# Performance work log

Measured on AMD Instinct MI355X. Metric: run time of the kernel, lower is better.

Reference implementation:

```python
import jax, jax.numpy as jnp
import numpy as np

B, C, S = 128, 32, 512          # batch, input_channel, seq_len (= d_model of the encoders)
EMB = 256                       # embed_size
NHEAD = 8                       # args.num_heads (also TransformerEncoderLayer nhead)
DFF = 2048                      # torch TransformerEncoderLayer default dim_feedforward
RLEN = S // 2 + 1               # 257 rfft bins
HK = int(RLEN * 0.5)            # 128, 'hight_freq_k' split point
LK = RLEN - HK                  # 129

def _ln(x, w, b, axes=-1):
    m = jnp.mean(x, axis=axes, keepdims=True)
    v = jnp.var(x, axis=axes, keepdims=True)
    return (x - m) / jnp.sqrt(v + 1e-5) * w + b

def _tel(x, in_w, in_b, out_w, out_b, ln1w, ln1b, w1, b1, w2, b2, ln2w, ln2b):
    # torch nn.TransformerEncoderLayer (batch_first, post-norm, relu, eval-mode dropout)
    b_, s_, d_ = x.shape
    dh = d_ // NHEAD
    qkv = x @ in_w.T + in_b
    q, k, v = jnp.split(qkv, 3, axis=-1)
    sp = lambda t: t.reshape(b_, s_, NHEAD, dh).transpose(0, 2, 1, 3)
    q, k, v = sp(q), sp(k), sp(v)
    sc = jnp.einsum('bhqd,bhkd->bhqk', q, k) / jnp.sqrt(jnp.asarray(dh, x.dtype))
    att = jax.nn.softmax(sc, axis=-1)
    o = jnp.einsum('bhqk,bhkd->bhqd', att, v).transpose(0, 2, 1, 3).reshape(b_, s_, d_)
    o = o @ out_w.T + out_b
    x = _ln(x + o, ln1w, ln1b)
    f = jax.nn.relu(x @ w1.T + b1) @ w2.T + b2
    return _ln(x + f, ln2w, ln2b)

def _crelu(z):
    return jax.lax.complex(jax.nn.relu(z.real), jax.nn.relu(z.imag))

def _csoftmax(z):
    return jax.lax.complex(jax.nn.softmax(z.real, axis=-1), jax.nn.softmax(z.imag, axis=-1))

def _cattn(q):
    # self-attention with complex Q=K=V (no conjugate, per torch matmul(Q, K^T))
    dk = q.shape[-1]
    sc = jnp.einsum('bqe,bke->bqk', q, q) / jnp.asarray(dk, jnp.float32) ** 0.5
    return jnp.einsum('bqk,bke->bqe', _csoftmax(sc), q)

def setup_inputs() -> dict:
    key = jax.random.key(0)
    ks = iter(jax.random.split(key, 64))
    n = lambda *sh: jax.random.normal(next(ks), sh, jnp.float32) * 0.02
    d = {'x': jax.random.normal(next(ks), (B, C, S), jnp.float32)}
    for p in ('t', 'r'):
        d[p + '_in_w'] = n(3 * S, S);  d[p + '_in_b'] = jnp.zeros((3 * S,), jnp.float32)
        d[p + '_out_w'] = n(S, S);     d[p + '_out_b'] = jnp.zeros((S,), jnp.float32)
        d[p + '_ln1_w'] = jnp.ones((S,), jnp.float32); d[p + '_ln1_b'] = jnp.zeros((S,), jnp.float32)
        d[p + '_lin1_w'] = n(DFF, S); d[p + '_lin1_b'] = jnp.zeros((DFF,), jnp.float32)
        d[p + '_lin2_w'] = n(S, DFF); d[p + '_lin2_b'] = jnp.zeros((S,), jnp.float32)
        d[p + '_ln2_w'] = jnp.ones((S,), jnp.float32); d[p + '_ln2_b'] = jnp.zeros((S,), jnp.float32)
    d['lc_w'] = n(S, S);  d['lc_b'] = jnp.zeros((S,), jnp.float32)
    d['up1_w'] = n(S, S); d['up1_b'] = jnp.zeros((S,), jnp.float32)
    d['up2_w'] = n(S, S); d['up2_b'] = jnp.zeros((S,), jnp.float32)
    d['n1_w'] = jnp.ones((C, S), jnp.float32); d['n1_b'] = jnp.zeros((C, S), jnp.float32)
    d['n2_w'] = jnp.ones((C, S), jnp.float32); d['n2_b'] = jnp.zeros((C, S), jnp.float32)
    d['l1_re'] = jax.random.normal(next(ks), (HK, EMB), jnp.float32)
    d['l1_im'] = jax.random.normal(next(ks), (HK, EMB), jnp.float32)
    d['h1_re'] = jax.random.normal(next(ks), (LK, EMB), jnp.float32)
    d['h1_im'] = jax.random.normal(next(ks), (LK, EMB), jnp.float32)
    d['lb1_re'] = jax.random.normal(next(ks), (EMB,), jnp.float32)
    d['lb1_im'] = jax.random.normal(next(ks), (EMB,), jnp.float32)
    d['hb1_re'] = jax.random.normal(next(ks), (EMB,), jnp.float32)
    d['hb1_im'] = jax.random.normal(next(ks), (EMB,), jnp.float32)
    return d

def reference(x, t_in_w, t_in_b, t_out_w, t_out_b, t_ln1_w, t_ln1_b, t_lin1_w, t_lin1_b, t_lin2_w, t_lin2_b, t_ln2_w, t_ln2_b, r_in_w, r_in_b, r_out_w, r_out_b, r_ln1_w, r_ln1_b, r_lin1_w, r_lin1_b, r_lin2_w, r_lin2_b, r_ln2_w, r_ln2_b, lc_w, lc_b, up1_w, up1_b, up2_w, up2_b, n1_w, n1_b, n2_w, n2_b, l1_re, l1_im, h1_re, h1_im, lb1_re, lb1_im, hb1_re, hb1_im):
    l1 = jax.lax.complex(l1_re, l1_im)
    h1 = jax.lax.complex(h1_re, h1_im)
    lb1 = jax.lax.complex(lb1_re, lb1_im)
    hb1 = jax.lax.complex(hb1_re, hb1_im)
    down_x = x  # downsample_scale=1 and padding_length=0 -> identity (i=0 path)
    # main branch
    df = jax.nn.relu(_tel(down_x, t_in_w, t_in_b, t_out_w, t_out_b, t_ln1_w, t_ln1_b,
                          t_lin1_w, t_lin1_b, t_lin2_w, t_lin2_b, t_ln2_w, t_ln2_b))
    df = _ln(df, n1_w, n1_b, axes=(-2, -1))
    # ttf_freqaug
    xf = jnp.fft.rfft(down_x, norm='ortho')                      # [B, C, 257] complex
    low = _crelu(jnp.einsum('bdk,ke->bde', xf[..., :HK], l1) + lb1)
    high = _crelu(jnp.einsum('bdk,ke->bde', xf[..., HK:], h1) + hb1)
    low = low + _cattn(low)
    high = high + _cattn(high)
    xcat = jnp.concatenate([low, high[..., low.shape[-1]:]], axis=-1)  # EMB bins (high slice is empty)
    fa = jnp.fft.irfft(xcat, n=S, norm='ortho')                  # zero-pads 256 -> 257 bins
    fa = fa @ lc_w.T + lc_b                                      # linear_change
    up = (fa @ up1_w.T + up1_b) @ up2_w.T + up2_b                # linear_up_sampling
    # recons branch
    rf = jax.nn.relu(_tel(fa, r_in_w, r_in_b, r_out_w, r_out_b, r_ln1_w, r_ln1_b,
                          r_lin1_w, r_lin1_b, r_lin2_w, r_lin2_b, r_ln2_w, r_ln2_b))
    rf = _ln(rf, n2_w, n2_b, axes=(-2, -1))
    res = df + rf
    return (res, down_x, fa, up)
```

## Files before the change

### kernel.cpp

```cpp
#include <hip/hip_runtime.h>
#include <math.h>


#define NROW 4096
#define NOUT 2097152

typedef __attribute__((ext_vector_type(8))) short short8;
typedef __attribute__((ext_vector_type(4))) float floatx4;

__device__ __forceinline__ unsigned short f2bf(float f) {
    union { float f; unsigned u; } v; v.f = f;
    return (unsigned short)((v.u + 0x7fffu + ((v.u >> 16) & 1u)) >> 16);
}
__device__ __forceinline__ float bf2f(unsigned short h) {
    union { unsigned u; float f; } v; v.u = ((unsigned)h) << 16;
    return v.f;
}

__device__ __forceinline__ void gload16(const unsigned short* g, unsigned short* l) {
    __builtin_amdgcn_global_load_lds((const __attribute__((address_space(1))) void*)g,
                                     (__attribute__((address_space(3))) void*)l, 16, 0, 0);
}

__device__ __forceinline__ void xcd_swizzle(int& bx, int& by, int& bz) {
    const int gx = gridDim.x, gy = gridDim.y;
    const int nwg = gx * gy * gridDim.z;
    int b = (bz * gy + by) * gx + bx;
    const int chunk = nwg >> 3;
    const int lb = (b & 7) * chunk + (b >> 3);
    bx = lb % gx;
    const int rem = lb / gx;
    by = rem % gy;
    bz = rem / gy;
}

__global__ __launch_bounds__(256) void tab_kernel(float* __restrict__ tabC, float* __restrict__ tabS)
{
    int n = blockIdx.x, k = threadIdx.x;
    int m = (n * k) & 511;
    float th = (float)m * 0.01227184630308513f;
    float s, c; sincosf(th, &s, &c);
    tabC[n * 256 + k] = c;
    tabS[n * 256 + k] = s;
}

__global__ __launch_bounds__(256) void wa_kernel(const float* __restrict__ l1_re, const float* __restrict__ l1_im,
                                                 const float* __restrict__ tabC, const float* __restrict__ tabS,
                                                 float* __restrict__ Wa)
{
    int n  = blockIdx.x;
    int ep = blockIdx.y * 256 + threadIdx.x;
    const float inv = 0.04419417382415922f;
    float acc = 0.f;
    if (ep < 256) {
        for (int k = 0; k < 128; ++k) {
            float c = tabC[n * 256 + k], s = tabS[n * 256 + k];
            acc += c * l1_re[k * 256 + ep] + s * l1_im[k * 256 + ep];
        }
    } else {
        int e = ep - 256;
        for (int k = 0; k < 128; ++k) {
            float c = tabC[n * 256 + k], s = tabS[n * 256 + k];
            acc += c * l1_im[k * 256 + e] - s * l1_re[k * 256 + e];
        }
    }
    Wa[(size_t)ep * 512 + n] = acc * inv;
}

__global__ __launch_bounds__(256) void wm_kernel(const float* __restrict__ lc_w,
                                                 const float* __restrict__ tabC, const float* __restrict__ tabS,
                                                 float* __restrict__ Wm)
{
    __shared__ float lw[512];
    int s  = blockIdx.x;
    int kk = blockIdx.y * 256 + threadIdx.x;
    for (int i = threadIdx.x; i < 512; i += 256) lw[i] = lc_w[s * 512 + i];
    __syncthreads();
    const float inv = 0.04419417382415922f;
    float acc = 0.f;
    if (kk < 256) {
        int k = kk;
        for (int n = 0; n < 512; ++n) acc += tabC[n * 256 + k] * lw[n];
        acc *= (k == 0) ? inv : 2.f * inv;
    } else {
        int k = kk - 256;
        if (k == 0) acc = 0.f;
        else {
            for (int n = 0; n < 512; ++n) acc += tabS[n * 256 + k] * lw[n];
            acc *= -2.f * inv;
        }
    }
    Wm[(size_t)s * 512 + kk] = acc;
}

__global__ __launch_bounds__(256) void lbpack_kernel(const float* __restrict__ re, const float* __restrict__ im,
                                                     float* __restrict__ out)
{
    int i = threadIdx.x + blockIdx.x * 256;
    if (i < 512) out[i] = (i < 256) ? re[i] : im[i - 256];
}

__global__ __launch_bounds__(256) void wcvt_kernel(
    const float* s0, const float* s1, const float* s2, const float* s3, const float* s4,
    const float* s5, const float* s6, const float* s7, const float* s8, const float* s9,
    unsigned short* __restrict__ o)
{
    int i = blockIdx.x * 256 + threadIdx.x;
    if (i >= 6815744) return;
    const float* s; int off;
    if (i < 3145728) {
        if (i < 1048576) { if (i < 786432) { s = s0; off = 0; } else { s = s1; off = 786432; } }
        else             { if (i < 2097152) { s = s2; off = 1048576; } else { s = s3; off = 2097152; } }
    } else {
        if (i < 5242880) {
            if (i < 3932160) { s = s4; off = 3145728; }
            else if (i < 4194304) { s = s5; off = 3932160; }
            else { s = s6; off = 4194304; }
        } else {
            if (i < 6291456) { s = s7; off = 5242880; }
            else if (i < 6553600) { s = s8; off = 6291456; }
            else { s = s9; off = 6553600; }
        }
    }
    o[i] = f2bf(s[i - off]);
}

__global__ __launch_bounds__(256) void cvt_hilo_kernel(const float* __restrict__ a, unsigned short* __restrict__ hi,
                                                       unsigned short* __restrict__ lo, int n)
{
    for (int i = blockIdx.x * 256 + threadIdx.x; i < n; i += gridDim.x * 256) {
        unsigned short h = f2bf(a[i]);
        hi[i] = h;
        lo[i] = f2bf(a[i] - bf2f(h));
    }
}
__global__ __launch_bounds__(256) void cvt_lo_kernel(const float* __restrict__ a, const unsigned short* __restrict__ hi,
                                                     unsigned short* __restrict__ lo, int n)
{
    for (int i = blockIdx.x * 256 + threadIdx.x; i < n; i += gridDim.x * 256)
        lo[i] = f2bf(a[i] - bf2f(hi[i]));
}

__global__ __launch_bounds__(256) void xsplit_kernel(const float* __restrict__ a, unsigned short* __restrict__ hi,
                                                     unsigned short* __restrict__ lo, float* __restrict__ cp, int n)
{
    for (int i = blockIdx.x * 256 + threadIdx.x; i < n; i += gridDim.x * 256) {
        float v = a[i];
        unsigned short h = f2bf(v);
        hi[i] = h;
        lo[i] = f2bf(v - bf2f(h));
        cp[i] = v;
    }
}

template <int TM, int TN, int ACT, int WF, int WBF>
__global__ __launch_bounds__(256) void gemm_mfma(
    const unsigned short* __restrict__ A, const unsigned short* __restrict__ W,
    const float* __restrict__ bias, float* __restrict__ Cf,
    unsigned short* __restrict__ Cb, int N, int K)
{
    constexpr int MI = TM / 32, NJ = TN / 32;
    constexpr int ARW = TM / 4, BRW = TN / 4;
    __shared__ unsigned short As[2][TM * 32];
    __shared__ unsigned short Bs[2][TN * 32];
    const int tid = threadIdx.x;
    const int wave = tid >> 6, lane = tid & 63;
    int bx = blockIdx.x, by = blockIdx.y, bz = blockIdx.z;
    xcd_swizzle(bx, by, bz);
    const int m0 = by * TM, n0 = bx * TN;
    const int sr = lane >> 2, sc = (lane & 3) * 8;
    const unsigned short* aS = A + (size_t)(m0 + wave * ARW + sr) * K + sc;
    const unsigned short* wS = W + (size_t)(n0 + wave * BRW + sr) * K + sc;
    const int wm = (wave >> 1) * (TM / 2), wn = (wave & 1) * (TN / 2);
    const int fr = lane & 15, fko = (lane >> 4) * 8;

    floatx4 acc[MI][NJ];
#pragma unroll
    for (int i = 0; i < MI; ++i)
#pragma unroll
        for (int j = 0; j < NJ; ++j) acc[i][j] = (floatx4){0.f, 0.f, 0.f, 0.f};

    for (int k0 = 0; k0 < K; k0 += 64) {
#pragma unroll
        for (int h = 0; h < 2; ++h) {
#pragma unroll
            for (int c = 0; c < ARW / 16; ++c)
                gload16(aS + (size_t)(16 * c) * K + k0 + 32 * h, &As[h][(wave * ARW + 16 * c) * 32]);
#pragma unroll
            for (int c = 0; c < BRW / 16; ++c)
                gload16(wS + (size_t)(16 * c) * K + k0 + 32 * h, &Bs[h][(wave * BRW + 16 * c) * 32]);
        }
        __syncthreads();
#pragma unroll
        for (int h = 0; h < 2; ++h) {
            short8 af[MI], bfr[NJ];
#pragma unroll
            for (int i = 0; i < MI; ++i) af[i] = *(const short8*)&As[h][(wm + i * 16 + fr) * 32 + fko];
#pragma unroll
            for (int j = 0; j < NJ; ++j) bfr[j] = *(const short8*)&Bs[h][(wn + j * 16 + fr) * 32 + fko];
#pragma unroll
            for (int i = 0; i < MI; ++i)
#pragma unroll
                for (int j = 0; j < NJ; ++j)
                    acc[i][j] = __builtin_amdgcn_mfma_f32_16x16x32_bf16(af[i], bfr[j], acc[i][j], 0, 0, 0);
        }
        __syncthreads();
    }
    const int r0 = m0 + wm + (lane >> 4) * 4;
#pragma unroll
    for (int i = 0; i < MI; ++i) {
#pragma unroll
        for (int j = 0; j < NJ; ++j) {
            int n = n0 + wn + j * 16 + fr;
            float bv = bias[n];
#pragma unroll
            for (int r = 0; r < 4; ++r) {
                int m = r0 + i * 16 + r;
                size_t idx = (size_t)m * N + n;
                float v = acc[i][j][r] + bv;
                if (ACT) v = fmaxf(v, 0.f);
                if (WF) Cf[idx] = v;
                if (WBF) Cb[idx] = f2bf(v);
            }
        }
    }
}

template <int TM, int TN, int ACT, int WBF>
__global__ __launch_bounds__(256) void gemm_dual(
    const unsigned short* __restrict__ A0, const unsigned short* __restrict__ A1,
    const unsigned short* __restrict__ W0, const unsigned short* __restrict__ W1,
    const float* __restrict__ b0, const float* __restrict__ b1,
    float* __restrict__ C0, float* __restrict__ C1,
    unsigned short* __restrict__ D0, unsigned short* __restrict__ D1, int N, int K)
{
    constexpr int MI = TM / 32, NJ = TN / 32;
    constexpr int ARW = TM / 4, BRW = TN / 4;
    __shared__ unsigned short As[2][TM * 32];
    __shared__ unsigned short Bs[2][TN * 32];
    const int tid = threadIdx.x;
    const int wave = tid >> 6, lane = tid & 63;
    int bx = blockIdx.x, by = blockIdx.y, bz = blockIdx.z;
    xcd_swizzle(bx, by, bz);
    const int m0 = by * TM, n0 = bx * TN;
    const int z = bz;
    const unsigned short* A = z ? A1 : A0;
    const unsigned short* W = z ? W1 : W0;
    const float* bias = z ? b1 : b0;
    float* Cf = z ? C1 : C0;
    unsigned short* Cb = z ? D1 : D0;
    const int sr = lane >> 2, sc = (lane & 3) * 8;
    const unsigned short* aS = A + (size_t)(m0 + wave * ARW + sr) * K + sc;
    const unsigned short* wS = W + (size_t)(n0 + wave * BRW + sr) * K + sc;
    const int wm = (wave >> 1) * (TM / 2), wn = (wave & 1) * (TN / 2);
    const int fr = lane & 15, fko = (lane >> 4) * 8;

    floatx4 acc[MI][NJ];
#pragma unroll
    for (int i = 0; i < MI; ++i)
#pragma unroll
        for (int j = 0; j < NJ; ++j) acc[i][j] = (floatx4){0.f, 0.f, 0.f, 0.f};

    for (int k0 = 0; k0 < K; k0 += 64) {
#pragma unroll
        for (int h = 0; h < 2; ++h) {
#pragma unroll
            for (int c = 0; c < ARW / 16; ++c)
                gload16(aS + (size_t)(16 * c) * K + k0 + 32 * h, &As[h][(wave * ARW + 16 * c) * 32]);
#pragma unroll
            for (int c = 0; c < BRW / 16; ++c)
                gload16(wS + (size_t)(16 * c) * K + k0 + 32 * h, &Bs[h][(wave * BRW + 16 * c) * 32]);
        }
        __syncthreads();
#pragma unroll
        for (int h = 0; h < 2; ++h) {
            short8 af[MI], bfr[NJ];
#pragma unroll
            for (int i = 0; i < MI; ++i) af[i] = *(const short8*)&As[h][(wm + i * 16 + fr) * 32 + fko];
#pragma unroll
            for (int j = 0; j < NJ; ++j) bfr[j] = *(const short8*)&Bs[h][(wn + j * 16 + fr) * 32 + fko];
#pragma unroll
            for (int i = 0; i < MI; ++i)
#pragma unroll
                for (int j = 0; j < NJ; ++j)
                    acc[i][j] = __builtin_amdgcn_mfma_f32_16x16x32_bf16(af[i], bfr[j], acc[i][j], 0, 0, 0);
        }
        __syncthreads();
    }
    const int r0 = m0 + wm + (lane >> 4) * 4;
#pragma unroll
    for (int i = 0; i < MI; ++i) {
#pragma unroll
        for (int j = 0; j < NJ; ++j) {
            int n = n0 + wn + j * 16 + fr;
            float bv = bias[n];
#pragma unroll
            for (int r = 0; r < 4; ++r) {
                int m = r0 + i * 16 + r;
                size_t idx = (size_t)m * N + n;
                float v = acc[i][j][r] + bv;
                if (ACT) v = fmaxf(v, 0.f);
                if (WBF) Cb[idx] = f2bf(v);
                else     Cf[idx] = v;
            }
        }
    }
}

template <int TM, int TN, int ACT, int WCOPY, int WHILO>
__global__ __launch_bounds__(256) void gemm_mfma3(
    const unsigned short* __restrict__ Ah, const unsigned short* __restrict__ Al,
    const unsigned short* __restrict__ Wh, const unsigned short* __restrict__ Wl,
    const float* __restrict__ bias, float* __restrict__ Cf, float* __restrict__ Ccopy,
    unsigned short* __restrict__ Hh, unsigned short* __restrict__ Hl, int N, int K)
{
    constexpr int MI = TM / 32, NJ = TN / 32;
    constexpr int ARW = TM / 4, BRW = TN / 4;
    __shared__ unsigned short Ash[2][TM * 32];
    __shared__ unsigned short Asl[2][TM * 32];
    __shared__ unsigned short Bsh[2][TN * 32];
    __shared__ unsigned short Bsl[2][TN * 32];
    const int tid = threadIdx.x;
    const int wave = tid >> 6, lane = tid & 63;
    int bx = blockIdx.x, by = blockIdx.y, bz = blockIdx.z;
    xcd_swizzle(bx, by, bz);
    const int m0 = by * TM, n0 = bx * TN;
    const int sr = lane >> 2, sc = (lane & 3) * 8;
    const size_t aoff = (size_t)(m0 + wave * ARW + sr) * K + sc;
    const size_t woff = (size_t)(n0 + wave * BRW + sr) * K + sc;
    const int wm = (wave >> 1) * (TM / 2), wn = (wave & 1) * (TN / 2);
    const int fr = lane & 15, fko = (lane >> 4) * 8;

    floatx4 acc[MI][NJ];
#pragma unroll
    for (int i = 0; i < MI; ++i)
#pragma unroll
        for (int j = 0; j < NJ; ++j) acc[i][j] = (floatx4){0.f, 0.f, 0.f, 0.f};

    for (int k0 = 0; k0 < K; k0 += 64) {
#pragma unroll
        for (int h = 0; h < 2; ++h) {
#pragma unroll
            for (int c = 0; c < ARW / 16; ++c) {
                gload16(Ah + aoff + (size_t)(16 * c) * K + k0 + 32 * h, &Ash[h][(wave * ARW + 16 * c) * 32]);
                gload16(Al + aoff + (size_t)(16 * c) * K + k0 + 32 * h, &Asl[h][(wave * ARW + 16 * c) * 32]);
            }
#pragma unroll
            for (int c = 0; c < BRW / 16; ++c) {
                gload16(Wh + woff + (size_t)(16 * c) * K + k0 + 32 * h, &Bsh[h][(wave * BRW + 16 * c) * 32]);
                gload16(Wl + woff + (size_t)(16 * c) * K + k0 + 32 * h, &Bsl[h][(wave * BRW + 16 * c) * 32]);
            }
        }
        __syncthreads();
#pragma unroll
        for (int h = 0; h < 2; ++h) {
            short8 ah[MI], al[MI], bh[NJ], bl[NJ];
#pragma unroll
            for (int i = 0; i < MI; ++i) {
                ah[i] = *(const short8*)&Ash[h][(wm + i * 16 + fr) * 32 + fko];
                al[i] = *(const short8*)&Asl[h][(wm + i * 16 + fr) * 32 + fko];
            }
#pragma unroll
            for (int j = 0; j < NJ; ++j) {
                bh[j] = *(const short8*)&Bsh[h][(wn + j * 16 + fr) * 32 + fko];
                bl[j] = *(const short8*)&Bsl[h][(wn + j * 16 + fr) * 32 + fko];
            }
#pragma unroll
            for (int i = 0; i < MI; ++i)
#pragma unroll
                for (int j = 0; j < NJ; ++j) {
                    acc[i][j] = __builtin_amdgcn_mfma_f32_16x16x32_bf16(al[i], bh[j], acc[i][j], 0, 0, 0);
                    acc[i][j] = __builtin_amdgcn_mfma_f32_16x16x32_bf16(ah[i], bl[j], acc[i][j], 0, 0, 0);
                    acc[i][j] = __builtin_amdgcn_mfma_f32_16x16x32_bf16(ah[i], bh[j], acc[i][j], 0, 0, 0);
                }
        }
        __syncthreads();
    }
    const int r0 = m0 + wm + (lane >> 4) * 4;
#pragma unroll
    for (int i = 0; i < MI; ++i) {
#pragma unroll
        for (int j = 0; j < NJ; ++j) {
            int n = n0 + wn + j * 16 + fr;
            float bv = bias[n];
#pragma unroll
            for (int r = 0; r < 4; ++r) {
                int m = r0 + i * 16 + r;
                size_t idx = (size_t)m * N + n;
                float v = acc[i][j][r] + bv;
                if (ACT) v = fmaxf(v, 0.f);
                Cf[idx] = v;
                if (WCOPY) Ccopy[idx] = v;
                if (WHILO) {
                    unsigned short h = f2bf(v);
                    Hh[idx] = h;
                    Hl[idx] = f2bf(v - bf2f(h));
                }
            }
        }
    }
}

__global__ __launch_bounds__(256) void attn_dual_kernel(const float* __restrict__ qkvF,
                                                        const unsigned short* __restrict__ qkvB,
                                                        unsigned short* __restrict__ outR,
                                                        unsigned short* __restrict__ outT)
{
    const int isT = blockIdx.x >> 10;
    const int bid = blockIdx.x & 1023;
    const int b = bid >> 3;
    const int h = bid & 7;
    __shared__ float qs[32][65], ks[32][65], vs[32][65];
    __shared__ float ps[32][33];
    const int tid = threadIdx.x;
    if (isT) {
        for (int i = tid; i < 2048; i += 256) {
            int s = i >> 6, d = i & 63;
            size_t base = ((size_t)(b * 32 + s)) * 1536 + h * 64 + d;
            qs[s][d] = bf2f(qkvB[base]);
            ks[s][d] = bf2f(qkvB[base + 512]);
            vs[s][d] = bf2f(qkvB[base + 1024]);
        }
    } else {
        for (int i = tid; i < 2048; i += 256) {
            int s = i >> 6, d = i & 63;
            size_t base = ((size_t)(b * 32 + s)) * 1536 + h * 64 + d;
            qs[s][d] = qkvF[base];
            ks[s][d] = qkvF[base + 512];
            vs[s][d] = qkvF[base + 1024];
        }
    }
    __syncthreads();
    for (int i = tid; i < 1024; i += 256) {
        int si = i >> 5, sj = i & 31;
        float acc = 0.f;
#pragma unroll 8
        for (int d = 0; d < 64; ++d) acc += qs[si][d] * ks[sj][d];
        ps[si][sj] = acc * 0.125f;
    }
    __syncthreads();
    if (tid < 32) {
        float mx = -1e30f;
        for (int j = 0; j < 32; ++j) mx = fmaxf(mx, ps[tid][j]);
        float sum = 0.f;
        for (int j = 0; j < 32; ++j) { float e = __expf(ps[tid][j] - mx); ps[tid][j] = e; sum += e; }
        float inv = 1.f / sum;
        for (int j = 0; j < 32; ++j) ps[tid][j] *= inv;
    }
    __syncthreads();
    unsigned short* ob = isT ? outT : outR;
    for (int i = tid; i < 2048; i += 256) {
        int s = i >> 6, d = i & 63;
        float acc = 0.f;
#pragma unroll 8
        for (int k = 0; k < 32; ++k) acc += ps[s][k] * vs[k][d];
        ob[((size_t)(b * 32 + s)) * 512 + h * 64 + d] = f2bf(acc);
    }
}

__global__ __launch_bounds__(512) void cattn2_kernel(const float* __restrict__ LL,
                                                     unsigned short* __restrict__ outHi,
                                                     unsigned short* __restrict__ outLo)
{
    extern __shared__ float Xs[];
    __shared__ float Pr[16][33], Pi[16][33];
    const int b = blockIdx.x, half = blockIdx.y;
    const int tid = threadIdx.x;
    const float* base = LL + (size_t)b * 16384;
    for (int i = tid; i < 16384; i += 512) {
        int c = i >> 9, e = i & 511;
        Xs[e * 32 + ((c ^ e) & 31)] = base[i];
    }
    __syncthreads();
    {
        const int li = tid >> 5;
        const int ci = half * 16 + li;
        const int ck = tid & 31;
        float ar = 0.f, ai = 0.f;
#pragma unroll 4
        for (int er = 0; er < 256; ++er) {
            const int sw = er & 31;
            float yr = Xs[er * 32 + ((ck ^ sw) & 31)];
            float yi = Xs[(er + 256) * 32 + ((ck ^ sw) & 31)];
            float xr = Xs[er * 32 + ((ci ^ sw) & 31)];
            float xi = Xs[(er + 256) * 32 + ((ci ^ sw) & 31)];
            ar += xr * yr - xi * yi;
            ai += xr * yi + xi * yr;
        }
        Pr[li][ck] = ar * 0.0625f;
        Pi[li][ck] = ai * 0.0625f;
    }
    __syncthreads();
    if (tid < 32) {
        int r = tid & 15;
        float (*P)[33] = (tid < 16) ? Pr : Pi;
        float mx = -1e30f;
        for (int j = 0; j < 32; ++j) mx = fmaxf(mx, P[r][j]);
        float s = 0.f;
        for (int j = 0; j < 32; ++j) { float e = __expf(P[r][j] - mx); P[r][j] = e; s += e; }
        float inv = 1.f / s;
        for (int j = 0; j < 32; ++j) P[r][j] *= inv;
    }
    __syncthreads();
    const int er = tid & 255;
    const int th = tid >> 8;
    const int sw = er & 31;
    float accr[8], acci[8];
#pragma unroll
    for (int t = 0; t < 8; ++t) { accr[t] = 0.f; acci[t] = 0.f; }
    for (int k = 0; k < 32; ++k) {
        float yr = Xs[er * 32 + ((k ^ sw) & 31)];
        float yi = Xs[(er + 256) * 32 + ((k ^ sw) & 31)];
#pragma unroll
        for (int t = 0; t < 8; ++t) {
            float pr = Pr[th * 8 + t][k], pi = Pi[th * 8 + t][k];
            accr[t] += pr * yr - pi * yi;
            acci[t] += pr * yi + pi * yr;
        }
    }
#pragma unroll
    for (int t = 0; t < 8; ++t) {
        int c = half * 16 + th * 8 + t;
        float vr = Xs[er * 32 + ((c ^ sw) & 31)] + accr[t];
        float vi = Xs[(er + 256) * 32 + ((c ^ sw) & 31)] + acci[t];
        size_t ir = (size_t)b * 16384 + (size_t)c * 512 + er;
        unsigned short hr = f2bf(vr), hi2 = f2bf(vi);
        outHi[ir] = hr;        outLo[ir] = f2bf(vr - bf2f(hr));
        outHi[ir + 256] = hi2; outLo[ir + 256] = f2bf(vi - bf2f(hi2));
    }
}

__global__ __launch_bounds__(256) void add_ln_d1(
    const float* __restrict__ r0, const float* __restrict__ y0,
    const float* __restrict__ w0, const float* __restrict__ b0,
    unsigned short* __restrict__ h0, unsigned short* __restrict__ l0,
    const float* __restrict__ r1, const float* __restrict__ y1,
    const float* __restrict__ w1, const float* __restrict__ b1,
    unsigned short* __restrict__ h1, unsigned short* __restrict__ l1)
{
    const int row = blockIdx.x;
    const int br = row >> 12;
    const int rl = row & 4095;
    const float* resid = br ? r1 : r0;
    const float* y     = br ? y1 : y0;
    const float* w     = br ? w1 : w0;
    const float* bb    = br ? b1 : b0;
    unsigned short* oh = br ? h1 : h0;
    unsigned short* ol = br ? l1 : l0;
    const int tid = threadIdx.x;
    const size_t base = (size_t)rl * 512;
    float v0 = resid[base + tid] + y[base + tid];
    float v1 = resid[base + 256 + tid] + y[base + 256 + tid];
    float s = v0 + v1, q = v0 * v0 + v1 * v1;
    for (int off = 32; off; off >>= 1) { s += __shfl_down(s, off); q += __shfl_down(q, off); }
    __shared__ float sw[4], qw[4], ms, is;
    int wid = tid >> 6, lane = tid & 63;
    if (lane == 0) { sw[wid] = s; qw[wid] = q; }
    __syncthreads();
    if (tid == 0) {
        float S = sw[0] + sw[1] + sw[2] + sw[3];
        float Q = qw[0] + qw[1] + qw[2] + qw[3];
        float m = S * (1.f / 512.f);
        ms = m;
        is = rsqrtf(Q * (1.f / 512.f) - m * m + 1e-5f);
    }
    __syncthreads();
    float m = ms, inv = is;
    float o0 = (v0 - m) * inv * w[tid] + bb[tid];
    float o1 = (v1 - m) * inv * w[256 + tid] + bb[256 + tid];
    unsigned short e0 = f2bf(o0), e1 = f2bf(o1);
    oh[base + tid] = e0;       ol[base + tid] = f2bf(o0 - bf2f(e0));
    oh[base + 256 + tid] = e1; ol[base + 256 + tid] = f2bf(o1 - bf2f(e1));
}

__global__ __launch_bounds__(256) void add_ln_d2(
    const unsigned short* __restrict__ rh0, const unsigned short* __restrict__ rl0,
    const float* __restrict__ y0, const float* __restrict__ w0, const float* __restrict__ b0,
    float* __restrict__ o0p,
    const unsigned short* __restrict__ rh1, const unsigned short* __restrict__ rl1,
    const float* __restrict__ y1, const float* __restrict__ w1, const float* __restrict__ b1,
    float* __restrict__ o1p)
{
    const int row = blockIdx.x;
    const int br = row >> 12;
    const int rl = row & 4095;
    const unsigned short* rh = br ? rh1 : rh0;
    const unsigned short* rlo = br ? rl1 : rl0;
    const float* y  = br ? y1 : y0;
    const float* w  = br ? w1 : w0;
    const float* bb = br ? b1 : b0;
    float* op = br ? o1p : o0p;
    const int tid = threadIdx.x;
    const size_t base = (size_t)rl * 512;
    float v0 = bf2f(rh[base + tid]) + bf2f(rlo[base + tid]) + y[base + tid];
    float v1 = bf2f(rh[base + 256 + tid]) + bf2f(rlo[base + 256 + tid]) + y[base + 256 + tid];
    float s = v0 + v1, q = v0 * v0 + v1 * v1;
    for (int off = 32; off; off >>= 1) { s += __shfl_down(s, off); q += __shfl_down(q, off); }
    __shared__ float sw[4], qw[4], ms, is;
    int wid = tid >> 6, lane = tid & 63;
    if (lane == 0) { sw[wid] = s; qw[wid] = q; }
    __syncthreads();
    if (tid == 0) {
        float S = sw[0] + sw[1] + sw[2] + sw[3];
        float Q = qw[0] + qw[1] + qw[2] + qw[3];
        float m = S * (1.f / 512.f);
        ms = m;
        is = rsqrtf(Q * (1.f / 512.f) - m * m + 1e-5f);
    }
    __syncthreads();
    float m = ms, inv = is;
    op[base + tid]       = (v0 - m) * inv * w[tid] + bb[tid];
    op[base + 256 + tid] = (v1 - m) * inv * w[256 + tid] + bb[256 + tid];
}

template <int ADDF>
__global__ __launch_bounds__(256) void relu_bln_kernel(const float* __restrict__ xin,
                                                       const float* __restrict__ w, const float* __restrict__ b,
                                                       const float* __restrict__ addsrc,
                                                       float* __restrict__ out)
{
    const int bb = blockIdx.x;
    const int tid = threadIdx.x;
    const float* xp = xin + (size_t)bb * 16384;
    float s = 0.f, q = 0.f;
    for (int i = tid; i < 16384; i += 256) { float v = fmaxf(xp[i], 0.f); s += v; q += v * v; }
    for (int off = 32; off; off >>= 1) { s += __shfl_down(s, off); q += __shfl_down(q, off); }
    __shared__ float sw[4], qw[4], ms, is;
    int wid = tid >> 6, lane = tid & 63;
    if (lane == 0) { sw[wid] = s; qw[wid] = q; }
    __syncthreads();
    if (tid == 0) {
        float S = sw[0] + sw[1] + sw[2] + sw[3];
        float Q = qw[0] + qw[1] + qw[2] + qw[3];
        float m = S * (1.f / 16384.f);
        ms = m;
        is = rsqrtf(Q * (1.f / 16384.f) - m * m + 1e-5f);
    }
    __syncthreads();
    float m = ms, inv = is;
    const float* ap = ADDF ? (addsrc + (size_t)bb * 16384) : nullptr;
    float* op = out + (size_t)bb * 16384;
    for (int i = tid; i < 16384; i += 256) {
        float v = fmaxf(xp[i], 0.f);
        float o = (v - m) * inv * w[i] + b[i];
        if (ADDF) o += ap[i];
        op[i] = o;
    }
}

extern "C" void kernel_launch(void* const* d_in, const int* in_sizes, int n_in,
                              void* d_out, int out_size, void* d_ws, size_t ws_size,
                              hipStream_t stream)
{
    (void)in_sizes; (void)n_in; (void)out_size; (void)ws_size;
    const float* x        = (const float*)d_in[0];
    const float* t_in_w   = (const float*)d_in[1];
    const float* t_in_b   = (const float*)d_in[2];
    const float* t_out_w  = (const float*)d_in[3];
    const float* t_out_b  = (const float*)d_in[4];
    const float* t_ln1_w  = (const float*)d_in[5];
    const float* t_ln1_b  = (const float*)d_in[6];
    const float* t_lin1_w = (const float*)d_in[7];
    const float* t_lin1_b = (const float*)d_in[8];
    const float* t_lin2_w = (const float*)d_in[9];
    const float* t_lin2_b = (const float*)d_in[10];
    const float* t_ln2_w  = (const float*)d_in[11];
    const float* t_ln2_b  = (const float*)d_in[12];
    const float* r_in_w   = (const float*)d_in[13];
    const float* r_in_b   = (const float*)d_in[14];
    const float* r_out_w  = (const float*)d_in[15];
    const float* r_out_b  = (const float*)d_in[16];
    const float* r_ln1_w  = (const float*)d_in[17];
    const float* r_ln1_b  = (const float*)d_in[18];
    const float* r_lin1_w = (const float*)d_in[19];
    const float* r_lin1_b = (const float*)d_in[20];
    const float* r_lin2_w = (const float*)d_in[21];
    const float* r_lin2_b = (const float*)d_in[22];
    const float* r_ln2_w  = (const float*)d_in[23];
    const float* r_ln2_b  = (const float*)d_in[24];
    const float* lc_w     = (const float*)d_in[25];
    const float* lc_b     = (const float*)d_in[26];
    const float* up1_w    = (const float*)d_in[27];
    const float* up1_b    = (const float*)d_in[28];
    const float* up2_w    = (const float*)d_in[29];
    const float* up2_b    = (const float*)d_in[30];
    const float* n1_w     = (const float*)d_in[31];
    const float* n1_b     = (const float*)d_in[32];
    const float* n2_w     = (const float*)d_in[33];
    const float* n2_b     = (const float*)d_in[34];
    const float* l1_re    = (const float*)d_in[35];
    const float* l1_im    = (const float*)d_in[36];
    const float* lb1_re   = (const float*)d_in[39];
    const float* lb1_im   = (const float*)d_in[40];

    float* outp = (float*)d_out;

    float* WS   = (float*)d_ws;
    float* LL   = WS;
    float* FA   = WS;
    float* yR   = WS;
    float* QR   = WS + 2097152;
    float* tabC = QR;
    float* tabS = QR + 131072;
    float* WaF  = QR + 262144;
    float* WmF  = QR + 524288;
    unsigned short* WaHu = (unsigned short*)(QR + 786432);
    unsigned short* WaLu = (unsigned short*)(QR + 917504);
    unsigned short* WmHu = (unsigned short*)(QR + 1048576);
    unsigned short* WmLu = (unsigned short*)(QR + 1179648);
    float* qkvR = QR;
    unsigned short* x1rH = (unsigned short*)(WS + 2097152);
    unsigned short* x1rL = (unsigned short*)(WS + 3145728);
    unsigned short* x1tH = (unsigned short*)(WS + 4194304);
    unsigned short* x1tL = (unsigned short*)(WS + 5242880);
    float* yT   = WS + 6291456;
    unsigned short* qkvT = (unsigned short*)(WS + 8388608);
    unsigned short* f1R  = (unsigned short*)(WS + 8388608);
    float* x2R  = WS + 8388608;
    float* x2T  = WS + 10485760;
    unsigned short* xHi = (unsigned short*)(WS + 11534336);
    unsigned short* xLo = (unsigned short*)(WS + 12582912);
    unsigned short* aoR = (unsigned short*)(WS + 11534336);
    unsigned short* aoT = (unsigned short*)(WS + 12582912);
    unsigned short* f1T = (unsigned short*)(WS + 12582912);
    unsigned short* LLH = (unsigned short*)(WS + 13631488);
    unsigned short* LLL = (unsigned short*)(WS + 14680064);
    unsigned short* u1b = (unsigned short*)(WS + 13631488);
    float* oR   = WS + 13631488;
    float* oT   = WS + 15728640;
    unsigned short* faHi = (unsigned short*)(WS + 15728640);
    unsigned short* faLo = (unsigned short*)(WS + 16777216);
    unsigned short* rinLoU = (unsigned short*)(WS + 17825792);
    float* LB   = WS + 18219008;
    unsigned short* WB = (unsigned short*)(WS + 18366464);

    unsigned short* w_tin  = WB + 0;
    unsigned short* w_tout = WB + 786432;
    unsigned short* w_tl1  = WB + 1048576;
    unsigned short* w_tl2  = WB + 2097152;
    unsigned short* w_rin  = WB + 3145728;
    unsigned short* w_rout = WB + 3932160;
    unsigned short* w_rl1  = WB + 4194304;
    unsigned short* w_rl2  = WB + 5242880;
    unsigned short* w_up1  = WB + 6291456;
    unsigned short* w_up2  = WB + 6553600;

    dim3 blk(256);

    tab_kernel<<<dim3(512), blk, 0, stream>>>(tabC, tabS);
    wa_kernel<<<dim3(512, 2), blk, 0, stream>>>(l1_re, l1_im, tabC, tabS, WaF);
    wm_kernel<<<dim3(512, 2), blk, 0, stream>>>(lc_w, tabC, tabS, WmF);
    cvt_hilo_kernel<<<dim3(1024), blk, 0, stream>>>(WaF, WaHu, WaLu, 262144);
    cvt_hilo_kernel<<<dim3(1024), blk, 0, stream>>>(WmF, WmHu, WmLu, 262144);
    lbpack_kernel<<<dim3(2), blk, 0, stream>>>(lb1_re, lb1_im, LB);
    wcvt_kernel<<<dim3(26624), blk, 0, stream>>>(t_in_w, t_out_w, t_lin1_w, t_lin2_w,
                                                 r_in_w, r_out_w, r_lin1_w, r_lin2_w,
                                                 up1_w, up2_w, WB);
    xsplit_kernel<<<dim3(2048), blk, 0, stream>>>(x, xHi, xLo, outp + NOUT, NOUT);

    gemm_mfma3<64,64,1,0,0><<<dim3(8, 64), blk, 0, stream>>>(xHi, xLo, WaHu, WaLu, LB,
                                                             LL, nullptr, nullptr, nullptr, 512, 512);
    cattn2_kernel<<<dim3(128, 2), dim3(512), 65536, stream>>>(LL, LLH, LLL);
    gemm_mfma3<64,64,0,1,1><<<dim3(8, 64), blk, 0, stream>>>(LLH, LLL, WmHu, WmLu, lc_b,
                                                             FA, outp + 2 * NOUT, faHi, faLo, 512, 512);
    cvt_lo_kernel<<<dim3(768), blk, 0, stream>>>(r_in_w, w_rin, rinLoU, 786432);

    gemm_mfma<64,64,0,0,1><<<dim3(8, 64), blk, 0, stream>>>(faHi, w_up1, up1_b, nullptr, u1b, 512, 512);
    gemm_mfma<64,64,0,1,0><<<dim3(8, 64), blk, 0, stream>>>(u1b, w_up2, up2_b, outp + 3 * NOUT, nullptr, 512, 512);

    gemm_mfma3<64,128,0,0,0><<<dim3(12, 64), blk, 0, stream>>>(faHi, faLo, w_rin, rinLoU, r_in_b,
                                                               qkvR, nullptr, nullptr, nullptr, 1536, 512);
    gemm_mfma<64,128,0,0,1><<<dim3(12, 64), blk, 0, stream>>>(xHi, w_tin, t_in_b, nullptr, qkvT, 1536, 512);

    attn_dual_kernel<<<dim3(2048), blk, 0, stream>>>(qkvR, qkvT, aoR, aoT);
    gemm_dual<64,64,0,0><<<dim3(8, 64, 2), blk, 0, stream>>>(aoR, aoT, w_rout, w_tout,
                                                             r_out_b, t_out_b, oR, oT,
                                                             nullptr, nullptr, 512, 512);
    add_ln_d1<<<dim3(8192), blk, 0, stream>>>(FA, oR, r_ln1_w, r_ln1_b, x1rH, x1rL,
                                              x,  oT, t_ln1_w, t_ln1_b, x1tH, x1tL);
    gemm_dual<64,128,1,1><<<dim3(16, 64, 2), blk, 0, stream>>>(x1rH, x1tH, w_rl1, w_tl1,
                                                               r_lin1_b, t_lin1_b, nullptr, nullptr,
                                                               f1R, f1T, 2048, 512);
    gemm_dual<64,64,0,0><<<dim3(8, 64, 2), blk, 0, stream>>>(f1R, f1T, w_rl2, w_tl2,
                                                             r_lin2_b, t_lin2_b, yR, yT,
                                                             nullptr, nullptr, 512, 2048);
    add_ln_d2<<<dim3(8192), blk, 0, stream>>>(x1rH, x1rL, yR, r_ln2_w, r_ln2_b, x2R,
                                              x1tH, x1tL, yT, t_ln2_w, t_ln2_b, x2T);
    relu_bln_kernel<0><<<dim3(128), blk, 0, stream>>>(x2R, n2_w, n2_b, nullptr, x2R);
    relu_bln_kernel<1><<<dim3(128), blk, 0, stream>>>(x2T, n1_w, n1_b, x2R, outp);
}
```

Baseline: 520.1 us.

## Fuse hi/lo bf16 split into weight-build kernels and enlarge dual GEMM tiles

The Wa and Wm precompute kernels now write bf16 hi/lo pairs directly, which removes two cvt_hilo launches and the fp32 intermediate round trip. Separately, the three gemm_dual calls switch from 64-row to 128-row M tiles with half the grid in y. This gives more data reuse per block but halves the block count, which may lower occupancy or load balance. The weight-build change also does strided 2-byte scattered stores instead of 4-byte ones.

```diff
diff --git a/kernel.cpp b/kernel.cpp
--- a/kernel.cpp
+++ b/kernel.cpp
@@ -46,7 +46,7 @@
 
 __global__ __launch_bounds__(256) void wa_kernel(const float* __restrict__ l1_re, const float* __restrict__ l1_im,
                                                  const float* __restrict__ tabC, const float* __restrict__ tabS,
-                                                 float* __restrict__ Wa)
+                                                 unsigned short* __restrict__ Wh, unsigned short* __restrict__ Wl)
 {
     int n  = blockIdx.x;
     int ep = blockIdx.y * 256 + threadIdx.x;
@@ -64,12 +64,16 @@
             acc += c * l1_im[k * 256 + e] - s * l1_re[k * 256 + e];
         }
     }
-    Wa[(size_t)ep * 512 + n] = acc * inv;
+    float v = acc * inv;
+    size_t idx = (size_t)ep * 512 + n;
+    unsigned short h = f2bf(v);
+    Wh[idx] = h;
+    Wl[idx] = f2bf(v - bf2f(h));
 }
 
 __global__ __launch_bounds__(256) void wm_kernel(const float* __restrict__ lc_w,
                                                  const float* __restrict__ tabC, const float* __restrict__ tabS,
-                                                 float* __restrict__ Wm)
+                                                 unsigned short* __restrict__ Wh, unsigned short* __restrict__ Wl)
 {
     __shared__ float lw[512];
     int s  = blockIdx.x;
@@ -90,7 +94,10 @@
             acc *= -2.f * inv;
         }
     }
-    Wm[(size_t)s * 512 + kk] = acc;
+    size_t idx = (size_t)s * 512 + kk;
+    unsigned short h = f2bf(acc);
+    Wh[idx] = h;
+    Wl[idx] = f2bf(acc - bf2f(h));
 }
 
 __global__ __launch_bounds__(256) void lbpack_kernel(const float* __restrict__ re, const float* __restrict__ im,
@@ -125,15 +132,6 @@
     o[i] = f2bf(s[i - off]);
 }
 
-__global__ __launch_bounds__(256) void cvt_hilo_kernel(const float* __restrict__ a, unsigned short* __restrict__ hi,
-                                                       unsigned short* __restrict__ lo, int n)
-{
-    for (int i = blockIdx.x * 256 + threadIdx.x; i < n; i += gridDim.x * 256) {
-        unsigned short h = f2bf(a[i]);
-        hi[i] = h;
-        lo[i] = f2bf(a[i] - bf2f(h));
-    }
-}
 __global__ __launch_bounds__(256) void cvt_lo_kernel(const float* __restrict__ a, const unsigned short* __restrict__ hi,
                                                      unsigned short* __restrict__ lo, int n)
 {
@@ -702,8 +700,6 @@
     float* QR   = WS + 2097152;
     float* tabC = QR;
     float* tabS = QR + 131072;
-    float* WaF  = QR + 262144;
-    float* WmF  = QR + 524288;
     unsigned short* WaHu = (unsigned short*)(QR + 786432);
     unsigned short* WaLu = (unsigned short*)(QR + 917504);
     unsigned short* WmHu = (unsigned short*)(QR + 1048576);
@@ -748,10 +744,8 @@
     dim3 blk(256);
 
     tab_kernel<<<dim3(512), blk, 0, stream>>>(tabC, tabS);
-    wa_kernel<<<dim3(512, 2), blk, 0, stream>>>(l1_re, l1_im, tabC, tabS, WaF);
-    wm_kernel<<<dim3(512, 2), blk, 0, stream>>>(lc_w, tabC, tabS, WmF);
-    cvt_hilo_kernel<<<dim3(1024), blk, 0, stream>>>(WaF, WaHu, WaLu, 262144);
-    cvt_hilo_kernel<<<dim3(1024), blk, 0, stream>>>(WmF, WmHu, WmLu, 262144);
+    wa_kernel<<<dim3(512, 2), blk, 0, stream>>>(l1_re, l1_im, tabC, tabS, WaHu, WaLu);
+    wm_kernel<<<dim3(512, 2), blk, 0, stream>>>(lc_w, tabC, tabS, WmHu, WmLu);
     lbpack_kernel<<<dim3(2), blk, 0, stream>>>(lb1_re, lb1_im, LB);
     wcvt_kernel<<<dim3(26624), blk, 0, stream>>>(t_in_w, t_out_w, t_lin1_w, t_lin2_w,
                                                  r_in_w, r_out_w, r_lin1_w, r_lin2_w,
@@ -773,17 +767,17 @@
     gemm_mfma<64,128,0,0,1><<<dim3(12, 64), blk, 0, stream>>>(xHi, w_tin, t_in_b, nullptr, qkvT, 1536, 512);
 
     attn_dual_kernel<<<dim3(2048), blk, 0, stream>>>(qkvR, qkvT, aoR, aoT);
-    gemm_dual<64,64,0,0><<<dim3(8, 64, 2), blk, 0, stream>>>(aoR, aoT, w_rout, w_tout,
-                                                             r_out_b, t_out_b, oR, oT,
-                                                             nullptr, nullptr, 512, 512);
+    gemm_dual<128,64,0,0><<<dim3(8, 32, 2), blk, 0, stream>>>(aoR, aoT, w_rout, w_tout,
+                                                              r_out_b, t_out_b, oR, oT,
+                                                              nullptr, nullptr, 512, 512);
     add_ln_d1<<<dim3(8192), blk, 0, stream>>>(FA, oR, r_ln1_w, r_ln1_b, x1rH, x1rL,
                                               x,  oT, t_ln1_w, t_ln1_b, x1tH, x1tL);
-    gemm_dual<64,128,1,1><<<dim3(16, 64, 2), blk, 0, stream>>>(x1rH, x1tH, w_rl1, w_tl1,
-                                                               r_lin1_b, t_lin1_b, nullptr, nullptr,
-                                                               f1R, f1T, 2048, 512);
-    gemm_dual<64,64,0,0><<<dim3(8, 64, 2), blk, 0, stream>>>(f1R, f1T, w_rl2, w_tl2,
-                                                             r_lin2_b, t_lin2_b, yR, yT,
-                                                             nullptr, nullptr, 512, 2048);
+    gemm_dual<128,128,1,1><<<dim3(16, 32, 2), blk, 0, stream>>>(x1rH, x1tH, w_rl1, w_tl1,
+                                                                r_lin1_b, t_lin1_b, nullptr, nullptr,
+                                                                f1R, f1T, 2048, 512);
+    gemm_dual<128,64,0,0><<<dim3(8, 32, 2), blk, 0, stream>>>(f1R, f1T, w_rl2, w_tl2,
+                                                              r_lin2_b, t_lin2_b, yR, yT,
+                                                              nullptr, nullptr, 512, 2048);
     add_ln_d2<<<dim3(8192), blk, 0, stream>>>(x1rH, x1rL, yR, r_ln2_w, r_ln2_b, x2R,
                                               x1tH, x1tL, yT, t_ln2_w, t_ln2_b, x2T);
     relu_bln_kernel<0><<<dim3(128), blk, 0, stream>>>(x2R, n2_w, n2_b, nullptr, x2R);
```

After: 523.9 us. Within noise of the previous version (+0.7%).
